# Optimization experiments

Measured on AMD Instinct MI355X. Metric: run time of the kernel, lower is better.

The kernel has to match this reference:

```python
import jax, jax.numpy as jnp
import numpy as np

M_TOKENS = 8192
K = 4096
N = 11008
BLOCK = 16
N_BLOCKS = K // BLOCK  # 256


def setup_inputs() -> dict:
    key = jax.random.key(0)
    k1, k2, k3, k4 = jax.random.split(key, 4)
    x = jax.random.normal(k1, (M_TOKENS, K), dtype=jnp.float16)
    # block-diagonal input rotations (DuQuant R_in), 16x16 per block
    R_in = jax.random.normal(k2, (N_BLOCKS, BLOCK, BLOCK), dtype=jnp.float16) * jnp.float16(0.25)
    # per-output-row scales (n_groups = 1, effective_group_size = in_features)
    scales = (jax.random.uniform(k3, (N, 1), dtype=jnp.float32) * 0.02 + 0.005).astype(jnp.float16)
    # symmetric uint4 zero point = 8.0
    zeros = jnp.full((N, 1), 8.0, dtype=jnp.float16)
    # input channel permutation (identity arange is a valid permutation)
    perm = jnp.arange(K, dtype=jnp.int32)
    # uint4 quantized weight values in [0, 15], stored unpacked
    qweight = jax.random.randint(k4, (N, K), 0, 16, dtype=jnp.int32)
    return {"x": x, "R_in": R_in, "scales": scales, "zeros": zeros,
            "perm": perm, "qweight": qweight}


def reference(x, R_in, scales, zeros, perm, qweight):
    # --- DuQuant input transform: permutation + block-diagonal rotation ---
    m = x.shape[0]
    xp = x[:, perm]                                   # [M, K]
    xb = xp.reshape(m, N_BLOCKS, BLOCK)               # [M, nb, 16]
    xt = jnp.einsum('mbi,bij->mbj', xb, R_in).reshape(m, K)  # [M, K] fp16
    # --- Dequantize uint4 weights: W = (q - zero) * scale, per output row ---
    Wd = (qweight.astype(jnp.float16) - zeros) * scales        # [N, K] fp16
    # --- W4A16 GEMM with fp32 accumulation, fp16 output ---
    y = jnp.einsum('mk,nk->mn', xt, Wd,
                   preferred_element_type=jnp.float32).astype(jnp.float16)
    return y
```

## Files before the change

kernel.cpp:

```cpp
#include <hip/hip_runtime.h>
#include <hip/hip_bf16.h>
#include <stdint.h>

#define M_TOK 8192
#define KDIM  4096
#define NDIM  11008

typedef float  f32x4  __attribute__((ext_vector_type(4)));
typedef int    i32x4  __attribute__((ext_vector_type(4)));
typedef unsigned short ushort8 __attribute__((ext_vector_type(8)));

__device__ __forceinline__ unsigned short f2b(float f) {
    union { float f; unsigned int i; } v; v.f = f;
    unsigned int u = v.i;
    unsigned int r = (u + 0x7fffu + ((u >> 16) & 1u)) >> 16;
    return (unsigned short)r;
}
__device__ __forceinline__ float b2f(unsigned short u) {
    union { unsigned int i; float f; } v; v.i = ((unsigned int)u) << 16; return v.f;
}

__device__ __forceinline__ void gl_lds16(const void* g, void* l) {
    __builtin_amdgcn_global_load_lds(
        (const __attribute__((address_space(1))) unsigned int*)g,
        (__attribute__((address_space(3))) unsigned int*)l, 16, 0, 0);
}

__global__ __launch_bounds__(256) void prep1_kernel(
    const float* __restrict__ x, const float* __restrict__ R,
    const int* __restrict__ perm, const int* __restrict__ qw,
    unsigned short* __restrict__ xt, float* __restrict__ pmax,
    signed char* __restrict__ q8)
{
    const int bid = blockIdx.x;
    const int t   = threadIdx.x;

    if (bid < 8192) {
        __shared__ float Rs[16 * 273];
        __shared__ int   ps[256];
        const int bg = bid & 15;
        const int mc = bid >> 4;

        ps[t] = perm[bg * 256 + t];
        {
            const float* Rg = R + (size_t)bg * 4096;
#pragma unroll
            for (int k = 0; k < 16; ++k) {
                const int idx = t * 16 + k;
                const int bs = idx >> 8;
                const int i  = (idx >> 4) & 15;
                const int j  = idx & 15;
                Rs[bs * 273 + i * 17 + j] = Rg[idx];
            }
        }
        __syncthreads();

        const int bs = t & 15;
        const int r  = t >> 4;
        const int m  = mc * 16 + r;
        const float* xrow = x + (size_t)m * KDIM;

        const int base = ps[bs * 16];
        bool contig = (base & 3) == 0;
#pragma unroll
        for (int i = 1; i < 16; ++i) contig &= (ps[bs * 16 + i] == base + i);

        float xv[16];
        if (contig) {
            const f32x4* xp = (const f32x4*)(xrow + base);
            const f32x4 a0 = xp[0], a1 = xp[1], a2 = xp[2], a3 = xp[3];
#pragma unroll
            for (int i = 0; i < 4; ++i) {
                xv[i]      = a0[i];
                xv[4 + i]  = a1[i];
                xv[8 + i]  = a2[i];
                xv[12 + i] = a3[i];
            }
        } else {
#pragma unroll
            for (int i = 0; i < 16; ++i) xv[i] = xrow[ps[bs * 16 + i]];
        }

        float o[16];
#pragma unroll
        for (int j = 0; j < 16; ++j) o[j] = 0.f;
#pragma unroll
        for (int i = 0; i < 16; ++i) {
            const float xi = xv[i];
            const float* Rrow = &Rs[bs * 273 + i * 17];
#pragma unroll
            for (int j = 0; j < 16; ++j) o[j] += xi * Rrow[j];
        }

        float lm = 0.f;
#pragma unroll
        for (int j = 0; j < 16; ++j) lm = fmaxf(lm, fabsf(o[j]));
#pragma unroll
        for (int k = 1; k < 16; k <<= 1) lm = fmaxf(lm, __shfl_xor(lm, k, 64));
        if (bs == 0) pmax[(size_t)m * 16 + bg] = lm;

        unsigned short os[16] __attribute__((aligned(16)));
#pragma unroll
        for (int j = 0; j < 16; ++j) os[j] = f2b(o[j]);
        unsigned short* dst = xt + (size_t)m * KDIM + bg * 256 + bs * 16;
        *(ushort8*)dst       = *(ushort8*)os;
        *(ushort8*)(dst + 8) = *(ushort8*)(os + 8);
    } else {
        const size_t base = ((size_t)(bid - 8192) * 256 + t) * 16;
        const int4* qp = (const int4*)(qw + base);
        signed char o[16] __attribute__((aligned(16)));
#pragma unroll
        for (int c = 0; c < 4; ++c) {
            const int4 v = qp[c];
            o[c*4+0] = (signed char)v.x; o[c*4+1] = (signed char)v.y;
            o[c*4+2] = (signed char)v.z; o[c*4+3] = (signed char)v.w;
        }
        *(int4*)(q8 + base) = *(const int4*)o;
    }
}

__global__ __launch_bounds__(256) void pack_kernel(
    const unsigned short* __restrict__ xt, const float* __restrict__ pmax,
    signed char* __restrict__ xt8, int* __restrict__ S, float* __restrict__ sa)
{
    const int m = blockIdx.x;
    const int t = threadIdx.x;

    float am = 1e-20f;
#pragma unroll
    for (int i = 0; i < 16; ++i) am = fmaxf(am, pmax[(size_t)m * 16 + i]);
    const float inv = 127.0f / am;

    const unsigned short* src = xt + (size_t)m * KDIM + t * 16;
    ushort8 u0 = *(const ushort8*)src;
    ushort8 u1 = *(const ushort8*)(src + 8);
    signed char qv[16] __attribute__((aligned(16)));
    int s = 0;
#pragma unroll
    for (int i = 0; i < 8; ++i) {
        int q0 = (int)rintf(b2f(u0[i]) * inv);
        q0 = q0 > 127 ? 127 : (q0 < -127 ? -127 : q0);
        qv[i] = (signed char)q0; s += q0;
        int q1 = (int)rintf(b2f(u1[i]) * inv);
        q1 = q1 > 127 ? 127 : (q1 < -127 ? -127 : q1);
        qv[8 + i] = (signed char)q1; s += q1;
    }
    *(int4*)(xt8 + (size_t)m * KDIM + t * 16) = *(const int4*)qv;

#pragma unroll
    for (int k = 1; k < 64; k <<= 1) s += __shfl_xor(s, k, 64);
    __shared__ int ws[4];
    if ((t & 63) == 0) ws[t >> 6] = s;
    __syncthreads();
    if (t == 0) {
        S[m]  = ws[0] + ws[1] + ws[2] + ws[3];
        sa[m] = am * (1.0f / 127.0f);
    }
}

#define BAR() do { asm volatile("" ::: "memory"); __builtin_amdgcn_s_barrier(); \
                   asm volatile("" ::: "memory"); } while (0)
#define WAITV(n) asm volatile("s_waitcnt vmcnt(" #n ")" ::: "memory")
#define PRIO1 __builtin_amdgcn_s_setprio(1)
#define PRIO0 __builtin_amdgcn_s_setprio(0)

#define ABASE(bb) ((bb)*32768)
#define BBASE(bb) ((bb)*32768 + 16384)

#define STAGE_A(bb, kB) do { \
    gl_lds16(aStageBase + (size_t)( 0)*KDIM + (kB), lds + ABASE(bb) +     0 + wOff); \
    gl_lds16(aStageBase + (size_t)(32)*KDIM + (kB), lds + ABASE(bb) +  4096 + wOff); \
    gl_lds16(aStageBase + (size_t)(64)*KDIM + (kB), lds + ABASE(bb) +  8192 + wOff); \
    gl_lds16(aStageBase + (size_t)(96)*KDIM + (kB), lds + ABASE(bb) + 12288 + wOff); \
} while (0)
#define STAGE_B(bb, kB) do { \
    gl_lds16(bStageBase + (size_t)( 0)*KDIM + (kB), lds + BBASE(bb) +     0 + wOff); \
    gl_lds16(bStageBase + (size_t)(32)*KDIM + (kB), lds + BBASE(bb) +  4096 + wOff); \
    gl_lds16(bStageBase + (size_t)(64)*KDIM + (kB), lds + BBASE(bb) +  8192 + wOff); \
    gl_lds16(bStageBase + (size_t)(96)*KDIM + (kB), lds + BBASE(bb) + 12288 + wOff); \
} while (0)

#define PH_READ_A(bb) do { \
    _Pragma("unroll") \
    for (int mf = 0; mf < 4; ++mf) { \
        aF[mf][0] = *(const i32x4*)(lds + ABASE(bb) + aRdBase + (mf*16)*128 + cs0); \
        aF[mf][1] = *(const i32x4*)(lds + ABASE(bb) + aRdBase + (mf*16)*128 + cs1); \
    } \
} while (0)
#define PH_READ_B(bb) do { \
    _Pragma("unroll") \
    for (int nf = 0; nf < 4; ++nf) { \
        bF[nf][0] = *(const i32x4*)(lds + BBASE(bb) + bRdBase + (nf*16)*128 + cs0); \
        bF[nf][1] = *(const i32x4*)(lds + BBASE(bb) + bRdBase + (nf*16)*128 + cs1); \
    } \
} while (0)

#define MFMA_H(h) do { \
    _Pragma("unroll") \
    for (int mf = 0; mf < 4; ++mf) \
    _Pragma("unroll") \
    for (int nf = 0; nf < 4; ++nf) \
        acc[mf][nf] = __builtin_amdgcn_mfma_i32_16x16x64_i8( \
            aF[mf][h], bF[nf][h], acc[mf][nf], 0, 0, 0); \
} while (0)

#define TILE(bb, kB, MODE) do { \
    PH_READ_A(bb); PH_READ_B(bb); \
    if ((MODE) <= 1) STAGE_B((bb)^1, (kB) + 128); \
    PRIO1; MFMA_H(0); PRIO0; \
    BAR(); \
    if ((MODE) == 0) STAGE_A(bb, (kB) + 256); \
    PRIO1; MFMA_H(1); PRIO0; \
    if ((MODE) == 0) WAITV(4); \
    if ((MODE) == 1) WAITV(0); \
    BAR(); \
} while (0)

__global__ __launch_bounds__(256, 2) void gemm_all(
    const signed char* __restrict__ Aq, const signed char* __restrict__ Bq,
    const float* __restrict__ sn, const float* __restrict__ zz,
    const float* __restrict__ sa, const int* __restrict__ S,
    float* __restrict__ C)
{
    __shared__ char lds[65536];

    const int tid  = threadIdx.x;
    const int wave = tid >> 6;
    const int lane = tid & 63;
    const int wr   = wave >> 1;
    const int wc   = wave & 1;
    const int wg   = blockIdx.x;

    const int swz = (wg & 7) * 688 + (wg >> 3);
    int tm, tn;
    if (swz < 5120) {
        const int Sx = swz >> 9;
        const int L  = swz & 511;
        tm = L >> 3;
        tn = (Sx << 3) + (L & 7);
    } else {
        const int L = swz - 5120;
        tm = L / 6;
        tn = 80 + (L - tm * 6);
    }

    const int sRow    = tid >> 3;
    const int gColSwz = (((tid & 7) ^ (sRow & 7)) << 4);
    const char* aStageBase = (const char*)Aq + (size_t)(tm * 128 + sRow) * KDIM + gColSwz;
    const char* bStageBase = (const char*)Bq + (size_t)(tn * 128 + sRow) * KDIM + gColSwz;
    const int wOff = wave * 1024;

    const int lane15 = lane & 15;
    const int lx  = (lane & 7) << 4;
    const int kq  = (lane >> 4) * 16;
    const int cs0 = kq ^ lx;
    const int cs1 = (kq + 64) ^ lx;
    const int aRdBase = wr * 8192 + lane15 * 128;
    const int bRdBase = wc * 8192 + lane15 * 128;

    i32x4 acc[4][4] = {};
    i32x4 aF[4][2];
    i32x4 bF[4][2];

    STAGE_A(0, 0);
    STAGE_B(0, 0);
    STAGE_A(1, 128);
    WAITV(4);
    BAR();

    int kB = 0;
#pragma unroll 1
    for (int t = 0; t < 29; t += 2) {
        TILE(0, kB, 0);
        TILE(1, kB + 128, 0);
        kB += 256;
    }
    TILE(0, 30 * 128, 1);
    TILE(1, 31 * 128, 2);

    const int row0 = tm * 128 + wr * 64 + (lane >> 4) * 4;
    const int col0 = tn * 128 + wc * 64 + lane15;
    float sn4[4], z4[4];
#pragma unroll
    for (int ni = 0; ni < 4; ++ni) { sn4[ni] = sn[col0 + ni*16]; z4[ni] = zz[col0 + ni*16]; }
#pragma unroll
    for (int mi = 0; mi < 4; ++mi) {
        const int rbase = row0 + mi * 16;
        float sa4[4], Sf4[4];
#pragma unroll
        for (int j = 0; j < 4; ++j) { sa4[j] = sa[rbase + j]; Sf4[j] = (float)S[rbase + j]; }
#pragma unroll
        for (int ni = 0; ni < 4; ++ni) {
            const i32x4 v = acc[mi][ni];
            const int c = col0 + ni * 16;
#pragma unroll
            for (int j = 0; j < 4; ++j)
                C[(size_t)(rbase + j) * NDIM + c] = sa4[j] * sn4[ni] * ((float)v[j] - z4[ni] * Sf4[j]);
        }
    }
}

extern "C" void kernel_launch(void* const* d_in, const int* in_sizes, int n_in,
                              void* d_out, int out_size, void* d_ws, size_t ws_size,
                              hipStream_t stream) {
    const float* x      = (const float*)d_in[0];
    const float* R      = (const float*)d_in[1];
    const float* scales = (const float*)d_in[2];
    const float* zeros  = (const float*)d_in[3];
    const int*   perm   = (const int*)d_in[4];
    const int*   qw     = (const int*)d_in[5];
    float*       out    = (float*)d_out;

    char* ws = (char*)d_ws;
    unsigned short* xt16 = (unsigned short*)ws;
    signed char*    xt8  = (signed char*)(ws + 67108864);
    signed char*    q8   = (signed char*)(ws + 100663296);
    float*          pmax = (float*)(ws + 145752064);
    float*          sa   = (float*)(ws + 146276352);
    int*            S    = (int*)(ws + 146309120);

    prep1_kernel<<<dim3(8192 + 11008), 256, 0, stream>>>(x, R, perm, qw, xt16, pmax, q8);
    pack_kernel<<<dim3(M_TOK), 256, 0, stream>>>(xt16, pmax, xt8, S, sa);
    gemm_all<<<dim3((M_TOK / 128) * (NDIM / 128)), 256, 0, stream>>>(xt8, q8, scales, zeros, sa, S, out);
}
```

Measured before the change: 458.2 us.

## Enlarge int8 GEMM tiles to 256x256 with a 128x256 tail path

Each workgroup's int8 GEMM tile grows from 128x128 to 256x256, so each wave now computes a 128x128 sub-tile of 8x8 MFMA fragments, which doubles operand reuse per LDS byte loaded. The LDS double buffer grows to 128 KB and launch bounds drop to one block per CU. The N remainder that does not fill a 256 tile is handled by a separate 128x256 tail path, and the block swizzle is rewritten for the new grid. The cost is much higher register pressure (about 256 accumulator registers per lane) and lower occupancy. The new grid also leaves a fractional last wave of workgroups across the CUs.

```diff
diff --git a/kernel.cpp b/kernel.cpp
--- a/kernel.cpp
+++ b/kernel.cpp
@@ -164,42 +164,42 @@
 #define PRIO1 __builtin_amdgcn_s_setprio(1)
 #define PRIO0 __builtin_amdgcn_s_setprio(0)
 
-#define ABASE(bb) ((bb)*32768)
-#define BBASE(bb) ((bb)*32768 + 16384)
-
-#define STAGE_A(bb, kB) do { \
-    gl_lds16(aStageBase + (size_t)( 0)*KDIM + (kB), lds + ABASE(bb) +     0 + wOff); \
-    gl_lds16(aStageBase + (size_t)(32)*KDIM + (kB), lds + ABASE(bb) +  4096 + wOff); \
-    gl_lds16(aStageBase + (size_t)(64)*KDIM + (kB), lds + ABASE(bb) +  8192 + wOff); \
-    gl_lds16(aStageBase + (size_t)(96)*KDIM + (kB), lds + ABASE(bb) + 12288 + wOff); \
-} while (0)
-#define STAGE_B(bb, kB) do { \
-    gl_lds16(bStageBase + (size_t)( 0)*KDIM + (kB), lds + BBASE(bb) +     0 + wOff); \
-    gl_lds16(bStageBase + (size_t)(32)*KDIM + (kB), lds + BBASE(bb) +  4096 + wOff); \
-    gl_lds16(bStageBase + (size_t)(64)*KDIM + (kB), lds + BBASE(bb) +  8192 + wOff); \
-    gl_lds16(bStageBase + (size_t)(96)*KDIM + (kB), lds + BBASE(bb) + 12288 + wOff); \
-} while (0)
+#define ABASE(bb) ((bb)*65536)
+#define BBASE(bb) ((bb)*65536 + 32768)
+
+#define STAGE8(basePtr, kB, ldsOff) do { \
+    gl_lds16(basePtr + (size_t)(  0)*KDIM + (kB), lds + (ldsOff) +     0 + wOff); \
+    gl_lds16(basePtr + (size_t)( 32)*KDIM + (kB), lds + (ldsOff) +  4096 + wOff); \
+    gl_lds16(basePtr + (size_t)( 64)*KDIM + (kB), lds + (ldsOff) +  8192 + wOff); \
+    gl_lds16(basePtr + (size_t)( 96)*KDIM + (kB), lds + (ldsOff) + 12288 + wOff); \
+    gl_lds16(basePtr + (size_t)(128)*KDIM + (kB), lds + (ldsOff) + 16384 + wOff); \
+    gl_lds16(basePtr + (size_t)(160)*KDIM + (kB), lds + (ldsOff) + 20480 + wOff); \
+    gl_lds16(basePtr + (size_t)(192)*KDIM + (kB), lds + (ldsOff) + 24576 + wOff); \
+    gl_lds16(basePtr + (size_t)(224)*KDIM + (kB), lds + (ldsOff) + 28672 + wOff); \
+} while (0)
+#define STAGE_A(bb, kB) STAGE8(aStageBase, kB, ABASE(bb))
+#define STAGE_B(bb, kB) STAGE8(bStageBase, kB, BBASE(bb))
 
 #define PH_READ_A(bb) do { \
     _Pragma("unroll") \
-    for (int mf = 0; mf < 4; ++mf) { \
-        aF[mf][0] = *(const i32x4*)(lds + ABASE(bb) + aRdBase + (mf*16)*128 + cs0); \
-        aF[mf][1] = *(const i32x4*)(lds + ABASE(bb) + aRdBase + (mf*16)*128 + cs1); \
+    for (int mf = 0; mf < 8; ++mf) { \
+        aF[mf][0] = *(const i32x4*)(lds + ABASE(bb) + aRdBase + mf*2048 + cs0); \
+        aF[mf][1] = *(const i32x4*)(lds + ABASE(bb) + aRdBase + mf*2048 + cs1); \
     } \
 } while (0)
 #define PH_READ_B(bb) do { \
     _Pragma("unroll") \
-    for (int nf = 0; nf < 4; ++nf) { \
-        bF[nf][0] = *(const i32x4*)(lds + BBASE(bb) + bRdBase + (nf*16)*128 + cs0); \
-        bF[nf][1] = *(const i32x4*)(lds + BBASE(bb) + bRdBase + (nf*16)*128 + cs1); \
+    for (int nf = 0; nf < 8; ++nf) { \
+        bF[nf][0] = *(const i32x4*)(lds + BBASE(bb) + bRdBase + nf*2048 + cs0); \
+        bF[nf][1] = *(const i32x4*)(lds + BBASE(bb) + bRdBase + nf*2048 + cs1); \
     } \
 } while (0)
 
 #define MFMA_H(h) do { \
     _Pragma("unroll") \
-    for (int mf = 0; mf < 4; ++mf) \
-    _Pragma("unroll") \
-    for (int nf = 0; nf < 4; ++nf) \
+    for (int mf = 0; mf < 8; ++mf) \
+    _Pragma("unroll") \
+    for (int nf = 0; nf < 8; ++nf) \
         acc[mf][nf] = __builtin_amdgcn_mfma_i32_16x16x64_i8( \
             aF[mf][h], bF[nf][h], acc[mf][nf], 0, 0, 0); \
 } while (0)
@@ -211,18 +211,65 @@
     BAR(); \
     if ((MODE) == 0) STAGE_A(bb, (kB) + 256); \
     PRIO1; MFMA_H(1); PRIO0; \
+    if ((MODE) == 0) WAITV(8); \
+    if ((MODE) == 1) WAITV(0); \
+    BAR(); \
+} while (0)
+
+#define TAB(bb) ((bb)*49152)
+#define TBB(bb) ((bb)*49152 + 16384)
+
+#define STAGE_TA(bb, kB) do { \
+    gl_lds16(aStageBase + (size_t)( 0)*KDIM + (kB), lds + TAB(bb) +     0 + wOff); \
+    gl_lds16(aStageBase + (size_t)(32)*KDIM + (kB), lds + TAB(bb) +  4096 + wOff); \
+    gl_lds16(aStageBase + (size_t)(64)*KDIM + (kB), lds + TAB(bb) +  8192 + wOff); \
+    gl_lds16(aStageBase + (size_t)(96)*KDIM + (kB), lds + TAB(bb) + 12288 + wOff); \
+} while (0)
+#define STAGE_TB(bb, kB) STAGE8(bStageBase, kB, TBB(bb))
+
+#define PH_READ_TA(bb) do { \
+    _Pragma("unroll") \
+    for (int mf = 0; mf < 4; ++mf) { \
+        aF[mf][0] = *(const i32x4*)(lds + TAB(bb) + aRdBase + mf*2048 + cs0); \
+        aF[mf][1] = *(const i32x4*)(lds + TAB(bb) + aRdBase + mf*2048 + cs1); \
+    } \
+} while (0)
+#define PH_READ_TB(bb) do { \
+    _Pragma("unroll") \
+    for (int nf = 0; nf < 8; ++nf) { \
+        bF[nf][0] = *(const i32x4*)(lds + TBB(bb) + bRdBase + nf*2048 + cs0); \
+        bF[nf][1] = *(const i32x4*)(lds + TBB(bb) + bRdBase + nf*2048 + cs1); \
+    } \
+} while (0)
+
+#define MFMA_TH(h) do { \
+    _Pragma("unroll") \
+    for (int mf = 0; mf < 4; ++mf) \
+    _Pragma("unroll") \
+    for (int nf = 0; nf < 8; ++nf) \
+        acc[mf][nf] = __builtin_amdgcn_mfma_i32_16x16x64_i8( \
+            aF[mf][h], bF[nf][h], acc[mf][nf], 0, 0, 0); \
+} while (0)
+
+#define TTILE(bb, kB, MODE) do { \
+    PH_READ_TA(bb); PH_READ_TB(bb); \
+    if ((MODE) <= 1) STAGE_TB((bb)^1, (kB) + 128); \
+    PRIO1; MFMA_TH(0); PRIO0; \
+    BAR(); \
+    if ((MODE) == 0) STAGE_TA(bb, (kB) + 256); \
+    PRIO1; MFMA_TH(1); PRIO0; \
     if ((MODE) == 0) WAITV(4); \
     if ((MODE) == 1) WAITV(0); \
     BAR(); \
 } while (0)
 
-__global__ __launch_bounds__(256, 2) void gemm_all(
+__global__ __launch_bounds__(256, 1) void gemm_all(
     const signed char* __restrict__ Aq, const signed char* __restrict__ Bq,
     const float* __restrict__ sn, const float* __restrict__ zz,
     const float* __restrict__ sa, const int* __restrict__ S,
     float* __restrict__ C)
 {
-    __shared__ char lds[65536];
+    __shared__ char lds[131072];
 
     const int tid  = threadIdx.x;
     const int wave = tid >> 6;
@@ -231,71 +278,119 @@
     const int wc   = wave & 1;
     const int wg   = blockIdx.x;
 
-    const int swz = (wg & 7) * 688 + (wg >> 3);
-    int tm, tn;
-    if (swz < 5120) {
-        const int Sx = swz >> 9;
-        const int L  = swz & 511;
-        tm = L >> 3;
-        tn = (Sx << 3) + (L & 7);
-    } else {
-        const int L = swz - 5120;
-        tm = L / 6;
-        tn = 80 + (L - tm * 6);
-    }
-
     const int sRow    = tid >> 3;
     const int gColSwz = (((tid & 7) ^ (sRow & 7)) << 4);
-    const char* aStageBase = (const char*)Aq + (size_t)(tm * 128 + sRow) * KDIM + gColSwz;
-    const char* bStageBase = (const char*)Bq + (size_t)(tn * 128 + sRow) * KDIM + gColSwz;
-    const int wOff = wave * 1024;
+    const int wOff    = wave * 1024;
 
     const int lane15 = lane & 15;
     const int lx  = (lane & 7) << 4;
     const int kq  = (lane >> 4) * 16;
     const int cs0 = kq ^ lx;
     const int cs1 = (kq + 64) ^ lx;
-    const int aRdBase = wr * 8192 + lane15 * 128;
-    const int bRdBase = wc * 8192 + lane15 * 128;
-
-    i32x4 acc[4][4] = {};
-    i32x4 aF[4][2];
-    i32x4 bF[4][2];
-
-    STAGE_A(0, 0);
-    STAGE_B(0, 0);
-    STAGE_A(1, 128);
-    WAITV(4);
-    BAR();
-
-    int kB = 0;
+
+    if (wg < 1280) {
+        const int swz = (wg & 7) * 160 + (wg >> 3);
+        const int Sx = swz >> 7;
+        const int L  = swz & 127;
+        const int tm = L >> 2;
+        const int tn = (Sx << 2) + (L & 3);
+
+        const char* aStageBase = (const char*)Aq + (size_t)(tm * 256 + sRow) * KDIM + gColSwz;
+        const char* bStageBase = (const char*)Bq + (size_t)(tn * 256 + sRow) * KDIM + gColSwz;
+
+        const int aRdBase = wr * 16384 + lane15 * 128;
+        const int bRdBase = wc * 16384 + lane15 * 128;
+
+        i32x4 acc[8][8] = {};
+        i32x4 aF[8][2];
+        i32x4 bF[8][2];
+
+        STAGE_A(0, 0);
+        STAGE_B(0, 0);
+        STAGE_A(1, 128);
+        WAITV(8);
+        BAR();
+
+        int kB = 0;
 #pragma unroll 1
-    for (int t = 0; t < 29; t += 2) {
-        TILE(0, kB, 0);
-        TILE(1, kB + 128, 0);
-        kB += 256;
-    }
-    TILE(0, 30 * 128, 1);
-    TILE(1, 31 * 128, 2);
-
-    const int row0 = tm * 128 + wr * 64 + (lane >> 4) * 4;
-    const int col0 = tn * 128 + wc * 64 + lane15;
-    float sn4[4], z4[4];
-#pragma unroll
-    for (int ni = 0; ni < 4; ++ni) { sn4[ni] = sn[col0 + ni*16]; z4[ni] = zz[col0 + ni*16]; }
-#pragma unroll
-    for (int mi = 0; mi < 4; ++mi) {
-        const int rbase = row0 + mi * 16;
-        float sa4[4], Sf4[4];
-#pragma unroll
-        for (int j = 0; j < 4; ++j) { sa4[j] = sa[rbase + j]; Sf4[j] = (float)S[rbase + j]; }
-#pragma unroll
-        for (int ni = 0; ni < 4; ++ni) {
-            const i32x4 v = acc[mi][ni];
-            const int c = col0 + ni * 16;
-#pragma unroll
-            for (int j = 0; j < 4; ++j)
-                C[(size_t)(rbase + j) * NDIM + c] = sa4[j] * sn4[ni] * ((float)v[j] - z4[ni] * Sf4[j]);
+        for (int t = 0; t < 29; t += 2) {
+            TILE(0, kB, 0);
+            TILE(1, kB + 128, 0);
+            kB += 256;
+        }
+        TILE(0, 30 * 128, 1);
+        TILE(1, 31 * 128, 2);
+
+        const int row0 = tm * 256 + wr * 128 + (lane >> 4) * 4;
+        const int col0 = tn * 256 + wc * 128 + lane15;
+        float sn8[8], z8[8];
+#pragma unroll
+        for (int ni = 0; ni < 8; ++ni) { sn8[ni] = sn[col0 + ni*16]; z8[ni] = zz[col0 + ni*16]; }
+#pragma unroll
+        for (int mi = 0; mi < 8; ++mi) {
+            const int rbase = row0 + mi * 16;
+            float sa4[4], Sf4[4];
+#pragma unroll
+            for (int j = 0; j < 4; ++j) { sa4[j] = sa[rbase + j]; Sf4[j] = (float)S[rbase + j]; }
+#pragma unroll
+            for (int ni = 0; ni < 8; ++ni) {
+                const i32x4 v = acc[mi][ni];
+                const int c = col0 + ni * 16;
+#pragma unroll
+                for (int j = 0; j < 4; ++j)
+                    C[(size_t)(rbase + j) * NDIM + c] = sa4[j] * sn8[ni] * ((float)v[j] - z8[ni] * Sf4[j]);
+            }
+        }
+    } else {
+        const int h   = wg - 1280;
+        const int tn  = 40 + (h % 3);
+        const int tmh = h / 3;
+
+        const char* aStageBase = (const char*)Aq + (size_t)(tmh * 128 + sRow) * KDIM + gColSwz;
+        const char* bStageBase = (const char*)Bq + (size_t)(tn * 256 + sRow) * KDIM + gColSwz;
+
+        const int aRdBase = wr * 8192 + lane15 * 128;
+        const int bRdBase = wc * 16384 + lane15 * 128;
+
+        i32x4 acc[4][8] = {};
+        i32x4 aF[4][2];
+        i32x4 bF[8][2];
+
+        STAGE_TA(0, 0);
+        STAGE_TB(0, 0);
+        STAGE_TA(1, 128);
+        WAITV(4);
+        BAR();
+
+        int kB = 0;
+#pragma unroll 1
+        for (int t = 0; t < 29; t += 2) {
+            TTILE(0, kB, 0);
+            TTILE(1, kB + 128, 0);
+            kB += 256;
+        }
+        TTILE(0, 30 * 128, 1);
+        TTILE(1, 31 * 128, 2);
+
+        const int row0 = tmh * 128 + wr * 64 + (lane >> 4) * 4;
+        const int col0 = tn * 256 + wc * 128 + lane15;
+        float sn8[8], z8[8];
+#pragma unroll
+        for (int ni = 0; ni < 8; ++ni) { sn8[ni] = sn[col0 + ni*16]; z8[ni] = zz[col0 + ni*16]; }
+#pragma unroll
+        for (int mi = 0; mi < 4; ++mi) {
+            const int rbase = row0 + mi * 16;
+            float sa4[4], Sf4[4];
+#pragma unroll
+            for (int j = 0; j < 4; ++j) { sa4[j] = sa[rbase + j]; Sf4[j] = (float)S[rbase + j]; }
+#pragma unroll
+            for (int ni = 0; ni < 8; ++ni) {
+                const i32x4 v = acc[mi][ni];
+                const int c = col0 + ni * 16;
+#pragma unroll
+                for (int j = 0; j < 4; ++j)
+                    C[(size_t)(rbase + j) * NDIM + c] = sa4[j] * sn8[ni] * ((float)v[j] - z8[ni] * Sf4[j]);
+            }
         }
     }
 }
@@ -321,5 +416,5 @@
 
     prep1_kernel<<<dim3(8192 + 11008), 256, 0, stream>>>(x, R, perm, qw, xt16, pmax, q8);
     pack_kernel<<<dim3(M_TOK), 256, 0, stream>>>(xt16, pmax, xt8, S, sa);
-    gemm_all<<<dim3((M_TOK / 128) * (NDIM / 128)), 256, 0, stream>>>(xt8, q8, scales, zeros, sa, S, out);
-}
+    gemm_all<<<dim3(1472), 256, 0, stream>>>(xt8, q8, scales, zeros, sa, S, out);
+}
```

Result: faster. 443.9 us (-3.1%).
